# Kernel tuning notes

Measured on AMD Instinct MI355X. Metric: run time of the kernel, lower is better.

The kernel has to match this reference:

```python
import jax, jax.numpy as jnp
import numpy as np

BATCH, IN_DIM, UNITS = 2048, 512, 512


def setup_inputs() -> dict:
    key = jax.random.key(0)
    k1, k2 = jax.random.split(key)
    x = jax.random.normal(k1, (BATCH, IN_DIM), dtype=jnp.float32)
    # He-style init for W, shape (1, in_dim, units) as in build()
    W = jax.random.normal(k2, (1, IN_DIM, UNITS), dtype=jnp.float32) * np.float32(np.sqrt(2.0 / IN_DIM))
    bias = jnp.zeros((UNITS,), dtype=jnp.float32)
    return {"x": x, "W": W, "bias": bias}


def reference(x, W, bias):
    # nodal 'exponential': exp(x * w) - 1, broadcast (batch,in,1)*(1,in,units)
    z = jnp.exp(x[:, :, None] * W) - 1.0          # (batch, in, units)
    # pool 'maximum': reduce over input dim
    p = jnp.max(z, axis=1)                         # (batch, units)
    # bias add + activation 'tanh'
    return jnp.tanh(p + bias)
```

## Files before the change

### kernel.cpp

```cpp
#include <hip/hip_runtime.h>


#define BATCH 2048
#define INDIM 512
#define UNITS 512

#define KC 32
#define RB 16
#define RG 8
#define NW 16

__global__ __launch_bounds__(1024, 8) void maxexp_kernel(
    const float* __restrict__ x,
    const float* __restrict__ W,
    const float* __restrict__ bias,
    float* __restrict__ out)
{
    __shared__ float part[RG][NW][64];

    const int f   = blockIdx.x;
    const int bg  = (f & 7) * 16 + ((f >> 3) & 15);
    const int ut  = f >> 7;

    const int lane = threadIdx.x & 63;
    const int wv   = __builtin_amdgcn_readfirstlane(threadIdx.x >> 6);
    const int u    = ut * 64 + lane;
    const int k0   = wv * KC;
    const int b0   = bg * RB;

    float wreg[KC];
    {
        const float* wp = W + (size_t)k0 * UNITS + u;
#pragma unroll
        for (int j = 0; j < KC; ++j) wreg[j] = wp[(size_t)j * UNITS];
    }
#pragma unroll
    for (int j = 0; j < KC; ++j) asm volatile("" : "+v"(wreg[j]));

    const float* xb = x + (size_t)b0 * INDIM + k0;
    const float bv  = bias[u];

#pragma unroll 1
    for (int g = 0; g < RB / RG; ++g) {
        float acc[RG];

#pragma unroll
        for (int t = 0; t < RG; ++t) {
            const float* xr = xb + (size_t)(g * RG + t) * INDIM;
            float c0 = -3.4e38f, c1 = -3.4e38f;
#pragma unroll
            for (int h = 0; h < 4; ++h) {
                const float4 a0 = *reinterpret_cast<const float4*>(xr +  0 + 4 * h);
                const float4 a1 = *reinterpret_cast<const float4*>(xr + 16 + 4 * h);
                const int j = 4 * h;
                c0 = fmaxf(fmaxf(c0, a0.x * wreg[ 0 + j]), a0.y * wreg[ 1 + j]);
                c0 = fmaxf(fmaxf(c0, a0.z * wreg[ 2 + j]), a0.w * wreg[ 3 + j]);
                c1 = fmaxf(fmaxf(c1, a1.x * wreg[16 + j]), a1.y * wreg[17 + j]);
                c1 = fmaxf(fmaxf(c1, a1.z * wreg[18 + j]), a1.w * wreg[19 + j]);
            }
            acc[t] = fmaxf(c0, c1);
        }

        __syncthreads();
#pragma unroll
        for (int t = 0; t < RG; ++t) part[t][wv][lane] = acc[t];
        __syncthreads();

        if (wv < RG) {
            const int t = wv;
            float m = -3.4e38f;
#pragma unroll
            for (int j = 0; j < NW; j += 2)
                m = fmaxf(fmaxf(m, part[t][j][lane]), part[t][j + 1][lane]);
            const float pp = __expf(m) - 1.0f + bv;
            const float e  = __expf(2.0f * pp);
            out[(size_t)(b0 + g * RG + t) * UNITS + u] = 1.0f - 2.0f / (e + 1.0f);
        }
    }
}

extern "C" void kernel_launch(void* const* d_in, const int* in_sizes, int n_in,
                              void* d_out, int out_size, void* d_ws, size_t ws_size,
                              hipStream_t stream) {
    const float* x    = (const float*)d_in[0];
    const float* W    = (const float*)d_in[1];
    const float* bias = (const float*)d_in[2];
    float* out = (float*)d_out;

    dim3 grid(BATCH / RB * (UNITS / 64));
    dim3 block(1024);
    maxexp_kernel<<<grid, block, 0, stream>>>(x, W, bias, out);
}
```

Baseline: 28.06 us.

## Use packed f32 multiplies with scalar x operands and single-pass reduction

```diff
diff --git a/kernel.cpp b/kernel.cpp
--- a/kernel.cpp
+++ b/kernel.cpp
@@ -7,8 +7,9 @@
 
 #define KC 32
 #define RB 16
-#define RG 8
 #define NW 16
+
+typedef float v2f __attribute__((ext_vector_type(2)));
 
 __global__ __launch_bounds__(1024, 8) void maxexp_kernel(
     const float* __restrict__ x,
@@ -16,7 +17,7 @@
     const float* __restrict__ bias,
     float* __restrict__ out)
 {
-    __shared__ float part[RG][NW][64];
+    __shared__ float part[RB][NW][64];
 
     const int f   = blockIdx.x;
     const int bg  = (f & 7) * 16 + ((f >> 3) & 15);
@@ -28,54 +29,51 @@
     const int k0   = wv * KC;
     const int b0   = bg * RB;
 
-    float wreg[KC];
+    v2f wp[KC / 2];
     {
-        const float* wp = W + (size_t)k0 * UNITS + u;
+        const float* wb = W + (size_t)k0 * UNITS + u;
 #pragma unroll
-        for (int j = 0; j < KC; ++j) wreg[j] = wp[(size_t)j * UNITS];
+        for (int j = 0; j < KC / 2; ++j) {
+            v2f t;
+            t.x = wb[(size_t)(2 * j)     * UNITS];
+            t.y = wb[(size_t)(2 * j + 1) * UNITS];
+            wp[j] = t;
+        }
     }
 #pragma unroll
-    for (int j = 0; j < KC; ++j) asm volatile("" : "+v"(wreg[j]));
+    for (int j = 0; j < KC / 2; ++j) asm("" : "+v"(wp[j]));
 
     const float* xb = x + (size_t)b0 * INDIM + k0;
-    const float bv  = bias[u];
 
-#pragma unroll 1
-    for (int g = 0; g < RB / RG; ++g) {
-        float acc[RG];
+    float acc[RB];
+#pragma unroll
+    for (int t = 0; t < RB; ++t) {
+        const v2f* xr = reinterpret_cast<const v2f*>(xb + (size_t)t * INDIM);
+        float m0 = -3.4e38f, m1 = -3.4e38f;
+#pragma unroll
+        for (int j = 0; j < KC / 2; j += 2) {
+            v2f p0, p1;
+            asm("v_pk_mul_f32 %0, %1, %2" : "=v"(p0) : "s"(xr[j]),     "v"(wp[j]));
+            asm("v_pk_mul_f32 %0, %1, %2" : "=v"(p1) : "s"(xr[j + 1]), "v"(wp[j + 1]));
+            m0 = fmaxf(fmaxf(m0, p0.x), p0.y);
+            m1 = fmaxf(fmaxf(m1, p1.x), p1.y);
+        }
+        acc[t] = fmaxf(m0, m1);
+    }
 
 #pragma unroll
-        for (int t = 0; t < RG; ++t) {
-            const float* xr = xb + (size_t)(g * RG + t) * INDIM;
-            float c0 = -3.4e38f, c1 = -3.4e38f;
+    for (int t = 0; t < RB; ++t) part[t][wv][lane] = acc[t];
+    __syncthreads();
+
+    {
+        const int t = wv;
+        float m = -3.4e38f;
 #pragma unroll
-            for (int h = 0; h < 4; ++h) {
-                const float4 a0 = *reinterpret_cast<const float4*>(xr +  0 + 4 * h);
-                const float4 a1 = *reinterpret_cast<const float4*>(xr + 16 + 4 * h);
-                const int j = 4 * h;
-                c0 = fmaxf(fmaxf(c0, a0.x * wreg[ 0 + j]), a0.y * wreg[ 1 + j]);
-                c0 = fmaxf(fmaxf(c0, a0.z * wreg[ 2 + j]), a0.w * wreg[ 3 + j]);
-                c1 = fmaxf(fmaxf(c1, a1.x * wreg[16 + j]), a1.y * wreg[17 + j]);
-                c1 = fmaxf(fmaxf(c1, a1.z * wreg[18 + j]), a1.w * wreg[19 + j]);
-            }
-            acc[t] = fmaxf(c0, c1);
-        }
-
-        __syncthreads();
-#pragma unroll
-        for (int t = 0; t < RG; ++t) part[t][wv][lane] = acc[t];
-        __syncthreads();
-
-        if (wv < RG) {
-            const int t = wv;
-            float m = -3.4e38f;
-#pragma unroll
-            for (int j = 0; j < NW; j += 2)
-                m = fmaxf(fmaxf(m, part[t][j][lane]), part[t][j + 1][lane]);
-            const float pp = __expf(m) - 1.0f + bv;
-            const float e  = __expf(2.0f * pp);
-            out[(size_t)(b0 + g * RG + t) * UNITS + u] = 1.0f - 2.0f / (e + 1.0f);
-        }
+        for (int j = 0; j < NW; j += 2)
+            m = fmaxf(fmaxf(m, part[t][j][lane]), part[t][j + 1][lane]);
+        const float pp = __expf(m) - 1.0f + bias[u];
+        const float e  = __expf(2.0f * pp);
+        out[(size_t)(b0 + t) * UNITS + u] = 1.0f - 2.0f / (e + 1.0f);
     }
 }
 
```

New measurement: 26.06 us. 1.08x faster.
